# Kernel tuning notes

Measured on AMD Instinct MI355X. Metric: run time of the kernel, lower is better.

Reference implementation:

```python
import jax, jax.numpy as jnp
import numpy as np

H, HK, D, WIN = 16, 4, 128, 1024  # n_head, n_kv_head, head_dim, left window


def rmsnorm(x):
    eps = jnp.asarray(jnp.finfo(x.dtype).eps, x.dtype)
    return x * jax.lax.rsqrt(jnp.mean(x * x, axis=-1, keepdims=True) + eps)


def rope(x, cos, sin):
    d = x.shape[-1] // 2
    x1, x2 = x[..., :d], x[..., d:]
    return jnp.concatenate([x1 * cos + x2 * sin, x1 * -sin + x2 * cos], axis=-1)


def setup_inputs() -> dict:
    key = jax.random.key(0)
    ks = jax.random.split(key, 12)
    B, T, C = 4, 2048, 2048
    t = jnp.arange(T, dtype=jnp.float32)[:, None]
    inv = 1.0 / (10000.0 ** (jnp.arange(D // 2, dtype=jnp.float32) / (D // 2)))
    ang = t * inv[None, :]  # [T, D/2]
    return {
        "x": jax.random.normal(ks[0], (B, T, C), jnp.float32),
        "x0": jax.random.normal(ks[1], (B, T, C), jnp.float32),
        "ve": jnp.zeros((B, T, C), jnp.float32),  # unused in add_init_qkv branch
        "cos": jnp.cos(ang)[None, :, None, :],  # [1,T,1,D/2]
        "sin": jnp.sin(ang)[None, :, None, :],
        "Wq": jax.random.normal(ks[2], (H * D, C), jnp.float32) * 0.02,
        "Wk": jax.random.normal(ks[3], (HK * D, C), jnp.float32) * 0.02,
        "Wv": jax.random.normal(ks[4], (HK * D, C), jnp.float32) * 0.02,
        "Wproj": jax.random.normal(ks[5], (C, H * D), jnp.float32) * 0.02,
        "alpha_q": jnp.ones((1,), jnp.float32),
        "beta_q": jax.random.uniform(ks[6], (1,), jnp.float32),
        "alpha_k": jnp.ones((1,), jnp.float32),
        "beta_k": jax.random.uniform(ks[7], (1,), jnp.float32),
        "alpha_v": jnp.ones((1,), jnp.float32),
        "beta_v": jax.random.uniform(ks[8], (1,), jnp.float32),
    }


def reference(x, x0, ve, cos, sin, Wq, Wk, Wv, Wproj,
              alpha_q, beta_q, alpha_k, beta_k, alpha_v, beta_v):
    B, T, C = x.shape
    g = H // HK  # GQA group size

    q = (x @ Wq.T).reshape(B, T, H, D)
    k = (x @ Wk.T).reshape(B, T, HK, D)
    v = (x @ Wv.T).reshape(B, T, HK, D)
    v_init = v

    # is_target + add_init_qkv + learn_init_coeffs: blend with projections of norm(x0)
    x0n = rmsnorm(x0)
    cqx = (x0n @ Wq.T).reshape(B, T, H, D)
    ckx = (x0n @ Wk.T).reshape(B, T, HK, D)
    cvx = (x0n @ Wv.T).reshape(B, T, HK, D)
    q = alpha_q * q + beta_q * cqx
    k = alpha_k * k + beta_k * ckx
    v = alpha_v * v + beta_v * cvx

    # rotary + qk-norm + 1.2 scale
    q = rmsnorm(rope(q, cos, sin)) * 1.2
    k = rmsnorm(rope(k, cos, sin)) * 1.2

    qg = q.reshape(B, T, HK, g, D)
    scale = 1.0 / np.sqrt(D)
    scores = jnp.einsum('bqhgd,bkhd->bhgqk', qg, k) * scale  # [B,HK,g,T,T]
    i = jnp.arange(T)[:, None]
    j = jnp.arange(T)[None, :]
    mask = (j <= i) & (i - j <= WIN)
    scores = jnp.where(mask, scores, -jnp.inf)
    p = jax.nn.softmax(scores, axis=-1)
    y = jnp.einsum('bhgqk,bkhd->bqhgd', p, v).reshape(B, T, H * D)

    y = y @ Wproj.T
    return (y, v_init)
```

## Files before the change

kernel.cpp:

```cpp
#include <hip/hip_runtime.h>
#include <hip/hip_bf16.h>
#include <math.h>


using bf16 = __hip_bfloat16;
typedef __attribute__((ext_vector_type(8))) short bf16x8;
typedef __attribute__((ext_vector_type(4))) short bf16x4;
typedef __attribute__((ext_vector_type(4))) float f32x4;

constexpr int Bb = 4, Ts = 2048, Cc = 2048, NH = 16, NKV = 4, Dh = 128, WIN = 1024;
constexpr float EPS = 1.1920929e-07f;

__device__ __forceinline__ void gld16(void* lds, const void* g) {
  __builtin_amdgcn_global_load_lds(
      (__attribute__((address_space(1))) unsigned int*)((void*)g),
      (__attribute__((address_space(3))) unsigned int*)lds, 16, 0, 0);
}

__device__ __forceinline__ unsigned short bfbits(float f) {
  bf16 h = __float2bfloat16(f);
  return __builtin_bit_cast(unsigned short, h);
}

__device__ __forceinline__ void store_out(float* p, float v) { *p = v; }
__device__ __forceinline__ void store_out(bf16* p, float v) { *p = __float2bfloat16(v); }

__device__ __forceinline__ f32x4 mfma16(bf16x4 a, bf16x4 b, f32x4 c) {
#if __has_builtin(__builtin_amdgcn_mfma_f32_16x16x16bf16_1k)
  return __builtin_amdgcn_mfma_f32_16x16x16bf16_1k(a, b, c, 0, 0, 0);
#else
  bf16x8 a8 = {a[0], a[1], a[2], a[3], 0, 0, 0, 0};
  bf16x8 b8 = {b[0], b[1], b[2], b[3], 0, 0, 0, 0};
  return __builtin_amdgcn_mfma_f32_16x16x32_bf16(a8, b8, c, 0, 0, 0);
#endif
}

__global__ __launch_bounds__(256) void convert_w4(
    const float* __restrict__ s0, bf16* __restrict__ d0,
    const float* __restrict__ s1, bf16* __restrict__ d1,
    const float* __restrict__ s2, bf16* __restrict__ d2,
    const float* __restrict__ s3, bf16* __restrict__ d3) {
  const int bid = blockIdx.x;
  const float* src;
  bf16* dst;
  int base;
  if (bid < 4096)      { src = s0; dst = d0; base = 0; }
  else if (bid < 5120) { src = s1; dst = d1; base = 4096; }
  else if (bid < 6144) { src = s2; dst = d2; base = 5120; }
  else                 { src = s3; dst = d3; base = 6144; }
  const int i = (bid - base) * 256 + threadIdx.x;
  float4 v = ((const float4*)src)[i];
  ushort4 u;
  u.x = bfbits(v.x); u.y = bfbits(v.y); u.z = bfbits(v.z); u.w = bfbits(v.w);
  ((ushort4*)dst)[i] = u;
}

__global__ __launch_bounds__(256) void prep(
    const float* __restrict__ x, const float* __restrict__ x0,
    const float* aq_p, const float* bq_p, const float* ak_p, const float* bk_p,
    bf16* __restrict__ xq, bf16* __restrict__ xk,
    bf16* __restrict__ xb, bf16* __restrict__ x0n) {
  const int row = blockIdx.x, tid = threadIdx.x;
  const float4* xr = (const float4*)(x + (size_t)row * Cc);
  const float4* nr = (const float4*)(x0 + (size_t)row * Cc);
  float4 xa[2], na[2];
  float ss = 0.f;
#pragma unroll
  for (int j = 0; j < 2; ++j) {
    xa[j] = xr[tid + j * 256];
    na[j] = nr[tid + j * 256];
    ss += na[j].x * na[j].x + na[j].y * na[j].y + na[j].z * na[j].z + na[j].w * na[j].w;
  }
#pragma unroll
  for (int o = 32; o; o >>= 1) ss += __shfl_xor(ss, o);
  __shared__ float red[4];
  if ((tid & 63) == 0) red[tid >> 6] = ss;
  __syncthreads();
  const float rms = rsqrtf((red[0] + red[1] + red[2] + red[3]) * (1.f / Cc) + EPS);
  const float aq = *aq_p, bq = *bq_p, ak = *ak_p, bk = *bk_p;
#pragma unroll
  for (int j = 0; j < 2; ++j) {
    const size_t base = (size_t)row * Cc + (size_t)(tid + j * 256) * 4;
    float nx[4] = {na[j].x * rms, na[j].y * rms, na[j].z * rms, na[j].w * rms};
    float xv[4] = {xa[j].x, xa[j].y, xa[j].z, xa[j].w};
    ushort4 uq, uk, ub, un;
    uq.x = bfbits(aq * xv[0] + bq * nx[0]); uq.y = bfbits(aq * xv[1] + bq * nx[1]);
    uq.z = bfbits(aq * xv[2] + bq * nx[2]); uq.w = bfbits(aq * xv[3] + bq * nx[3]);
    uk.x = bfbits(ak * xv[0] + bk * nx[0]); uk.y = bfbits(ak * xv[1] + bk * nx[1]);
    uk.z = bfbits(ak * xv[2] + bk * nx[2]); uk.w = bfbits(ak * xv[3] + bk * nx[3]);
    ub.x = bfbits(xv[0]); ub.y = bfbits(xv[1]); ub.z = bfbits(xv[2]); ub.w = bfbits(xv[3]);
    un.x = bfbits(nx[0]); un.y = bfbits(nx[1]); un.z = bfbits(nx[2]); un.w = bfbits(nx[3]);
    *(ushort4*)(xq + base) = uq;
    *(ushort4*)(xk + base) = uk;
    *(ushort4*)(xb + base) = ub;
    *(ushort4*)(x0n + base) = un;
  }
}

template <typename OutT>
__device__ __forceinline__ void gemm_body(
    const bf16* __restrict__ A, const bf16* __restrict__ W,
    OutT* __restrict__ C, int N, int K) {
  __shared__ unsigned short sA[128 * 64];
  __shared__ unsigned short sB[128 * 64];
  const int tid = threadIdx.x, wave = tid >> 6, lane = tid & 63;
  const int quad = lane >> 4, l15 = lane & 15;
  const int bm = blockIdx.x * 128, bn = blockIdx.y * 128;
  const int wm = (wave >> 1) * 64, wn = (wave & 1) * 64;
  const int srow = wave * 32 + (lane >> 3);
  const int scol = (lane & 7) * 8;

  f32x4 acc[4][4] = {};

  for (int k0 = 0; k0 < K; k0 += 64) {
#pragma unroll
    for (int i = 0; i < 4; ++i) {
      gld16(&sA[(wave * 32 + i * 8) * 64], &A[(size_t)(bm + srow + i * 8) * K + k0 + scol]);
      gld16(&sB[(wave * 32 + i * 8) * 64], &W[(size_t)(bn + srow + i * 8) * K + k0 + scol]);
    }
    __syncthreads();
#pragma unroll
    for (int kk = 0; kk < 2; ++kk) {
      bf16x8 af[4], bfr[4];
#pragma unroll
      for (int t = 0; t < 4; ++t)
        af[t] = *(const bf16x8*)&sA[(wm + t * 16 + l15) * 64 + kk * 32 + quad * 8];
#pragma unroll
      for (int t = 0; t < 4; ++t)
        bfr[t] = *(const bf16x8*)&sB[(wn + t * 16 + l15) * 64 + kk * 32 + quad * 8];
#pragma unroll
      for (int tm = 0; tm < 4; ++tm)
#pragma unroll
        for (int tn = 0; tn < 4; ++tn)
          acc[tm][tn] = __builtin_amdgcn_mfma_f32_16x16x32_bf16(af[tm], bfr[tn], acc[tm][tn], 0, 0, 0);
    }
    __syncthreads();
  }
#pragma unroll
  for (int tm = 0; tm < 4; ++tm)
#pragma unroll
    for (int tn = 0; tn < 4; ++tn)
#pragma unroll
      for (int r = 0; r < 4; ++r) {
        const int row = bm + wm + tm * 16 + quad * 4 + r;
        const int col = bn + wn + tn * 16 + l15;
        store_out(&C[(size_t)row * N + col], acc[tm][tn][r]);
      }
}

template <typename OutT>
__global__ __launch_bounds__(256) void gemm_bt(
    const bf16* __restrict__ A, const bf16* __restrict__ W,
    OutT* __restrict__ C, int N, int K) {
  gemm_body<OutT>(A, W, C, N, K);
}

struct GemmTriple { const bf16* A; const bf16* W; bf16* C; };
struct GemmTriple3 { GemmTriple t[3]; };

__global__ __launch_bounds__(256) void gemm_bt3(GemmTriple3 g, int N, int K) {
  const GemmTriple tr = g.t[blockIdx.z];
  gemm_body<bf16>(tr.A, tr.W, tr.C, N, K);
}

__global__ __launch_bounds__(256) void post_qk2(
    const bf16* __restrict__ qpre, const bf16* __restrict__ kpre,
    const float* __restrict__ cosp, const float* __restrict__ sinp,
    bf16* __restrict__ qh, bf16* __restrict__ kh, float qmult) {
  int bid = blockIdx.x;
  const bf16* pre;
  bf16* outh;
  int nh;
  float mult;
  if (bid < 32768) { pre = qpre; outh = qh; nh = NH; mult = qmult; }
  else { bid -= 32768; pre = kpre; outh = kh; nh = NKV; mult = 1.2f; }
  const int wid = bid * 4 + (threadIdx.x >> 6);
  const int lane = threadIdx.x & 63;
  const int h = wid % nh;
  const int bt = wid / nh;
  const int t = bt & (Ts - 1);
  const int b = bt >> 11;
  const size_t src = (size_t)bt * (size_t)(nh * Dh) + (size_t)h * Dh;
  float x1 = __bfloat162float(pre[src + lane]);
  float x2 = __bfloat162float(pre[src + 64 + lane]);
  float c = cosp[t * 64 + lane], s = sinp[t * 64 + lane];
  float o1 = x1 * c + x2 * s;
  float o2 = x2 * c - x1 * s;
  float ss = o1 * o1 + o2 * o2;
#pragma unroll
  for (int o = 32; o; o >>= 1) ss += __shfl_xor(ss, o);
  const float r = rsqrtf(ss * (1.f / Dh) + EPS) * mult;
  const size_t dst = ((size_t)(b * nh + h) * Ts + t) * Dh;
  outh[dst + lane] = __float2bfloat16(o1 * r);
  outh[dst + 64 + lane] = __float2bfloat16(o2 * r);
}

__global__ __launch_bounds__(256) void post_v(
    const bf16* __restrict__ vinit, const bf16* __restrict__ cvx,
    const float* av_p, const float* bv_p,
    bf16* __restrict__ vth, float* __restrict__ vout) {
  __shared__ unsigned short vt[128 * 65];
  const int t0 = blockIdx.x * 64;
  const int b = blockIdx.y >> 2, hk = blockIdx.y & 3;
  const float av = *av_p, bv = *bv_p;
  const int tid = threadIdx.x;
  for (int j = 0; j < 32; ++j) {
    const int e = j * 256 + tid;
    const int tl = e >> 7, d = e & 127;
    const size_t src = (size_t)(b * Ts + t0 + tl) * (NKV * Dh) + hk * Dh + d;
    const float vi = __bfloat162float(vinit[src]);
    const float cv = __bfloat162float(cvx[src]);
    vout[src] = vi;
    vt[d * 65 + tl] = bfbits(av * vi + bv * cv);
  }
  __syncthreads();
#pragma unroll
  for (int j = 0; j < 4; ++j) {
    const int g = j * 256 + tid;
    const int d = g >> 3, t8 = (g & 7) * 8;
    const unsigned short* p = &vt[d * 65 + t8];
    uint4 u;
    u.x = p[0] | ((unsigned int)p[1] << 16);
    u.y = p[2] | ((unsigned int)p[3] << 16);
    u.z = p[4] | ((unsigned int)p[5] << 16);
    u.w = p[6] | ((unsigned int)p[7] << 16);
    *(uint4*)&vth[((size_t)(b * NKV + hk) * Dh + d) * Ts + t0 + t8] = u;
  }
}

__global__ __launch_bounds__(256) void attn(
    const bf16* __restrict__ qh, const bf16* __restrict__ kh,
    const bf16* __restrict__ vth, bf16* __restrict__ att) {
  __shared__ unsigned short sK[64 * 128];
  __shared__ unsigned short sV[128 * 64];

  const int tid = threadIdx.x, wave = tid >> 6, lane = tid & 63;
  const int quad = lane >> 4, l15 = lane & 15;
  const int lin = blockIdx.y * 16 + blockIdx.x;
  const int swz = (lin & 7) * 128 + (lin >> 3);
  const int q0 = (swz & 15) * 128;
  const int by = swz >> 4;
  const int b = by >> 4, h = by & 15, hk = h >> 2;

  const bf16* Qp = qh + (size_t)(b * NH + h) * Ts * Dh;
  const bf16* Kp = kh + (size_t)(b * NKV + hk) * Ts * Dh;
  const bf16* Vp = vth + (size_t)(b * NKV + hk) * Dh * Ts;

  const int qw = q0 + wave * 32;

  bf16x8 qf[2][4];
#pragma unroll
  for (int tm = 0; tm < 2; ++tm)
#pragma unroll
    for (int kk = 0; kk < 4; ++kk)
      qf[tm][kk] = *(const bf16x8*)&Qp[(size_t)(qw + tm * 16 + l15) * Dh + kk * 32 + quad * 8];

  f32x4 of[2][8] = {};
  f32x4 l4[2] = {};

  const int krow = lane >> 4, kgp = lane & 15;
  const int vrow = lane >> 3, vgp = lane & 7;

  const int jt_lo = q0 >= WIN ? (q0 - WIN) >> 6 : 0;
  const int jt_hi = (q0 + 127) >> 6;

  for (int jt = jt_lo; jt <= jt_hi; ++jt) {
    const int j0 = jt << 6;
    __syncthreads();
#pragma unroll
    for (int i = 0; i < 4; ++i) {
      const int row = wave * 16 + i * 4 + krow;
      gld16(&sK[(wave * 16 + i * 4) * 128],
            &Kp[(size_t)(j0 + row) * Dh + (kgp ^ (row & 15)) * 8]);
      const int d = wave * 32 + i * 8 + vrow;
      gld16(&sV[(wave * 32 + i * 8) * 64],
            &Vp[(size_t)d * Ts + j0 + (vgp ^ (d & 7)) * 8]);
    }
    __syncthreads();

    if (j0 > qw + 31 || qw > j0 + 63 + WIN) continue;

    const bool full = (j0 + 63 <= qw) && (qw + 31 - j0 <= WIN);

#pragma unroll
    for (int tn = 0; tn < 4; ++tn) {
      f32x4 s[2] = {};
#pragma unroll
      for (int kk = 0; kk < 4; ++kk) {
        const bf16x8 kf = *(const bf16x8*)&sK[(tn * 16 + l15) * 128 + (((kk * 4 + quad) ^ l15) * 8)];
#pragma unroll
        for (int tm = 0; tm < 2; ++tm)
          s[tm] = __builtin_amdgcn_mfma_f32_16x16x32_bf16(kf, qf[tm][kk], s[tm], 0, 0, 0);
      }
      bf16x4 pf[2];
#pragma unroll
      for (int tm = 0; tm < 2; ++tm) {
        if (!full) {
          const int dq = (qw + tm * 16 + l15) - (j0 + tn * 16 + quad * 4);
#pragma unroll
          for (int r = 0; r < 4; ++r)
            if ((unsigned)(dq - r) > (unsigned)WIN) s[tm][r] = -__builtin_inff();
        }
#pragma unroll
        for (int r = 0; r < 4; ++r) {
          const float p = __builtin_amdgcn_exp2f(s[tm][r]);
          l4[tm][r] += p;
          pf[tm][r] = (short)bfbits(p);
        }
      }
      const int gsw = (tn * 2) ^ (l15 & 7);
#pragma unroll
      for (int dn = 0; dn < 8; ++dn) {
        const int d = dn * 16 + l15;
        const bf16x4 vf = *(const bf16x4*)&sV[d * 64 + ((gsw ^ (quad >> 1)) * 8) + (quad & 1) * 4];
        of[0][dn] = mfma16(pf[0], vf, of[0][dn]);
        of[1][dn] = mfma16(pf[1], vf, of[1][dn]);
      }
    }
  }

#pragma unroll
  for (int tm = 0; tm < 2; ++tm) {
    float l = (l4[tm][0] + l4[tm][1]) + (l4[tm][2] + l4[tm][3]);
    l += __shfl_xor(l, 16);
    l += __shfl_xor(l, 32);
#pragma unroll
    for (int r = 0; r < 4; ++r) {
      const float lr = __shfl(l, quad * 4 + r);
      const float inv = 1.f / lr;
      const int qr = qw + tm * 16 + quad * 4 + r;
      bf16* dst = att + (size_t)(b * Ts + qr) * (NH * Dh) + h * Dh;
#pragma unroll
      for (int dn = 0; dn < 8; ++dn)
        dst[dn * 16 + l15] = __float2bfloat16(of[tm][dn][r] * inv);
    }
  }
}

extern "C" void kernel_launch(void* const* d_in, const int* in_sizes, int n_in,
                              void* d_out, int out_size, void* d_ws, size_t ws_size,
                              hipStream_t stream) {
  const float* x = (const float*)d_in[0];
  const float* x0 = (const float*)d_in[1];
  const float* cosp = (const float*)d_in[3];
  const float* sinp = (const float*)d_in[4];
  const float* Wq = (const float*)d_in[5];
  const float* Wk = (const float*)d_in[6];
  const float* Wv = (const float*)d_in[7];
  const float* Wp = (const float*)d_in[8];
  const float* aq = (const float*)d_in[9];
  const float* bq = (const float*)d_in[10];
  const float* ak = (const float*)d_in[11];
  const float* bk = (const float*)d_in[12];
  const float* av = (const float*)d_in[13];
  const float* bv = (const float*)d_in[14];

  char* ws = (char*)d_ws;
  const size_t MB = 1024ull * 1024;
  bf16* xq = (bf16*)(ws + 0 * MB);
  bf16* xk = (bf16*)(ws + 32 * MB);
  bf16* xb = (bf16*)(ws + 64 * MB);
  bf16* x0n = (bf16*)(ws + 96 * MB);
  bf16* vinit = (bf16*)(ws + 128 * MB);
  bf16* cvx = (bf16*)(ws + 136 * MB);
  bf16* Wqb = (bf16*)(ws + 144 * MB);
  bf16* Wkb = (bf16*)(ws + 152 * MB);
  bf16* Wvb = (bf16*)(ws + 154 * MB);
  bf16* Wpb = (bf16*)(ws + 156 * MB);
  bf16* att = xq;
  bf16* qh = xk;
  bf16* kh = xb;
  bf16* vth = (bf16*)(ws + 72 * MB);

  float* y = (float*)d_out;
  float* vout = (float*)d_out + (size_t)Bb * Ts * Cc;
  bf16* q_pre = (bf16*)d_out;
  bf16* k_pre = (bf16*)vout;

  convert_w4<<<10240, 256, 0, stream>>>(Wq, Wqb, Wk, Wkb, Wv, Wvb, Wp, Wpb);

  prep<<<8192, 256, 0, stream>>>(x, x0, aq, bq, ak, bk, xq, xk, xb, x0n);

  gemm_bt<bf16><<<dim3(64, 16), 256, 0, stream>>>(xq, Wqb, q_pre, 2048, 2048);

  GemmTriple3 g3;
  g3.t[0] = {xk, Wkb, k_pre};
  g3.t[1] = {xb, Wvb, vinit};
  g3.t[2] = {x0n, Wvb, cvx};
  gemm_bt3<<<dim3(64, 4, 3), 256, 0, stream>>>(g3, 512, 2048);

  const float qmult = 1.2f * 0.08838834764831845f * 1.4426950408889634f;
  post_qk2<<<40960, 256, 0, stream>>>(q_pre, k_pre, cosp, sinp, qh, kh, qmult);
  post_v<<<dim3(32, 16), 256, 0, stream>>>(vinit, cvx, av, bv, vth, vout);

  attn<<<dim3(16, 64), 256, 0, stream>>>(qh, kh, vth, att);

  gemm_bt<float><<<dim3(64, 16), 256, 0, stream>>>(att, Wpb, y, 2048, 2048);
}
```

Measured before the change: 735.9 us.

## Use 256x256 double-buffered swizzled GEMM tiles with 512-thread blocks

Replaces the 128x128 single-buffered GEMM body with a 256x256 tile computed by 8 waves. It double-buffers LDS via async global-to-LDS loads with explicit vmcnt waits, and XOR-swizzles LDS columns to avoid bank conflicts. The goal is more data reuse per byte loaded, overlap of loads with MFMA work, and fewer LDS conflicts. In exchange it uses 128KB of LDS, limiting occupancy to one block per CU, and grids shrink to about one wave of blocks, which risks tail imbalance for the smaller GEMMs.

```diff
diff --git a/kernel.cpp b/kernel.cpp
--- a/kernel.cpp
+++ b/kernel.cpp
@@ -98,46 +98,72 @@
 }
 
 template <typename OutT>
-__device__ __forceinline__ void gemm_body(
+__device__ __forceinline__ void gemm256_body(
     const bf16* __restrict__ A, const bf16* __restrict__ W,
-    OutT* __restrict__ C, int N, int K) {
-  __shared__ unsigned short sA[128 * 64];
-  __shared__ unsigned short sB[128 * 64];
+    OutT* __restrict__ C, int N, int K, int bm, int bn) {
+  __shared__ unsigned short sA[2][256 * 64];
+  __shared__ unsigned short sB[2][256 * 64];
   const int tid = threadIdx.x, wave = tid >> 6, lane = tid & 63;
   const int quad = lane >> 4, l15 = lane & 15;
-  const int bm = blockIdx.x * 128, bn = blockIdx.y * 128;
-  const int wm = (wave >> 1) * 64, wn = (wave & 1) * 64;
-  const int srow = wave * 32 + (lane >> 3);
-  const int scol = (lane & 7) * 8;
-
-  f32x4 acc[4][4] = {};
-
-  for (int k0 = 0; k0 < K; k0 += 64) {
+  const int wm = (wave >> 2) * 128, wn = (wave & 3) * 64;
+  const int srow8 = lane >> 3;
+  const int sg = lane & 7;
+
+  f32x4 acc[8][4] = {};
+  const int nt = K >> 6;
+
+  auto stage = [&](int t, int buf) {
+    const int k0 = t << 6;
 #pragma unroll
     for (int i = 0; i < 4; ++i) {
-      gld16(&sA[(wave * 32 + i * 8) * 64], &A[(size_t)(bm + srow + i * 8) * K + k0 + scol]);
-      gld16(&sB[(wave * 32 + i * 8) * 64], &W[(size_t)(bn + srow + i * 8) * K + k0 + scol]);
-    }
-    __syncthreads();
+      const int row = i * 64 + wave * 8 + srow8;
+      const int swz = (sg ^ (row & 7)) * 8;
+      gld16(&sA[buf][(i * 64 + wave * 8) * 64],
+            &A[(size_t)(bm + row) * K + k0 + swz]);
+      gld16(&sB[buf][(i * 64 + wave * 8) * 64],
+            &W[(size_t)(bn + row) * K + k0 + swz]);
+    }
+  };
+
+  stage(0, 0);
+  stage(1, 1);
+  asm volatile("s_waitcnt vmcnt(8)" ::: "memory");
+  __builtin_amdgcn_sched_barrier(0);
+  __builtin_amdgcn_s_barrier();
+
+  for (int t = 0; t < nt; ++t) {
+    const unsigned short* a = sA[t & 1];
+    const unsigned short* w = sB[t & 1];
 #pragma unroll
     for (int kk = 0; kk < 2; ++kk) {
-      bf16x8 af[4], bfr[4];
-#pragma unroll
-      for (int t = 0; t < 4; ++t)
-        af[t] = *(const bf16x8*)&sA[(wm + t * 16 + l15) * 64 + kk * 32 + quad * 8];
-#pragma unroll
-      for (int t = 0; t < 4; ++t)
-        bfr[t] = *(const bf16x8*)&sB[(wn + t * 16 + l15) * 64 + kk * 32 + quad * 8];
-#pragma unroll
-      for (int tm = 0; tm < 4; ++tm)
+      const int gsw = ((kk * 4 + quad) ^ (l15 & 7)) * 8;
+      bf16x8 af[8], bfr[4];
+#pragma unroll
+      for (int i = 0; i < 8; ++i)
+        af[i] = *(const bf16x8*)&a[(wm + i * 16 + l15) * 64 + gsw];
+#pragma unroll
+      for (int i = 0; i < 4; ++i)
+        bfr[i] = *(const bf16x8*)&w[(wn + i * 16 + l15) * 64 + gsw];
+#pragma unroll
+      for (int tm = 0; tm < 8; ++tm)
 #pragma unroll
         for (int tn = 0; tn < 4; ++tn)
           acc[tm][tn] = __builtin_amdgcn_mfma_f32_16x16x32_bf16(af[tm], bfr[tn], acc[tm][tn], 0, 0, 0);
     }
-    __syncthreads();
-  }
-#pragma unroll
-  for (int tm = 0; tm < 4; ++tm)
+    if (t == nt - 1) break;
+    __builtin_amdgcn_s_barrier();
+    if (t + 2 < nt) {
+      stage(t + 2, t & 1);
+      asm volatile("s_waitcnt vmcnt(8)" ::: "memory");
+    } else {
+      asm volatile("s_waitcnt vmcnt(0)" ::: "memory");
+    }
+    __builtin_amdgcn_sched_barrier(0);
+    __builtin_amdgcn_s_barrier();
+  }
+
+#pragma unroll
+  for (int tm = 0; tm < 8; ++tm)
 #pragma unroll
     for (int tn = 0; tn < 4; ++tn)
 #pragma unroll
@@ -149,18 +175,18 @@
 }
 
 template <typename OutT>
-__global__ __launch_bounds__(256) void gemm_bt(
+__global__ __launch_bounds__(512) void gemm_bt(
     const bf16* __restrict__ A, const bf16* __restrict__ W,
     OutT* __restrict__ C, int N, int K) {
-  gemm_body<OutT>(A, W, C, N, K);
+  gemm256_body<OutT>(A, W, C, N, K, blockIdx.x * 256, blockIdx.y * 256);
 }
 
 struct GemmTriple { const bf16* A; const bf16* W; bf16* C; };
 struct GemmTriple3 { GemmTriple t[3]; };
 
-__global__ __launch_bounds__(256) void gemm_bt3(GemmTriple3 g, int N, int K) {
+__global__ __launch_bounds__(512) void gemm_bt3(GemmTriple3 g, int N, int K) {
   const GemmTriple tr = g.t[blockIdx.z];
-  gemm_body<bf16>(tr.A, tr.W, tr.C, N, K);
+  gemm256_body<bf16>(tr.A, tr.W, tr.C, N, K, blockIdx.x * 256, blockIdx.y * 256);
 }
 
 __global__ __launch_bounds__(256) void post_qk2(
@@ -381,13 +407,13 @@
 
   prep<<<8192, 256, 0, stream>>>(x, x0, aq, bq, ak, bk, xq, xk, xb, x0n);
 
-  gemm_bt<bf16><<<dim3(64, 16), 256, 0, stream>>>(xq, Wqb, q_pre, 2048, 2048);
+  gemm_bt<bf16><<<dim3(32, 8), 512, 0, stream>>>(xq, Wqb, q_pre, 2048, 2048);
 
   GemmTriple3 g3;
   g3.t[0] = {xk, Wkb, k_pre};
   g3.t[1] = {xb, Wvb, vinit};
   g3.t[2] = {x0n, Wvb, cvx};
-  gemm_bt3<<<dim3(64, 4, 3), 256, 0, stream>>>(g3, 512, 2048);
+  gemm_bt3<<<dim3(32, 2, 3), 512, 0, stream>>>(g3, 512, 2048);
 
   const float qmult = 1.2f * 0.08838834764831845f * 1.4426950408889634f;
   post_qk2<<<40960, 256, 0, stream>>>(q_pre, k_pre, cosp, sinp, qh, kh, qmult);
@@ -395,5 +421,5 @@
 
   attn<<<dim3(16, 64), 256, 0, stream>>>(qh, kh, vth, att);
 
-  gemm_bt<float><<<dim3(64, 16), 256, 0, stream>>>(att, Wpb, y, 2048, 2048);
-}
+  gemm_bt<float><<<dim3(32, 8), 512, 0, stream>>>(att, Wpb, y, 2048, 2048);
+}
```

Measured after the change: 653.4 us. 1.13x faster.
